# Kernel optimization log

Hardware: AMD Instinct MI355X
Metric: run time of the kernel (lower is better)

The kernel has to match this reference:

```python
import jax, jax.numpy as jnp
import numpy as np

N_NODES = 100000
N_EDGES = 1600000
IN_DIM = 768
HIDDEN = 256
N_CLASSES = 3


def setup_inputs() -> dict:
    key = jax.random.key(0)
    k0, k1, k2, k3 = jax.random.split(key, 4)
    x = jax.random.normal(k0, (N_NODES, IN_DIM), dtype=jnp.float32)
    edge_index = jax.random.randint(k1, (2, N_EDGES), 0, N_NODES, dtype=jnp.int32)
    # Glorot-ish init for weights
    W1 = jax.random.normal(k2, (IN_DIM, HIDDEN), dtype=jnp.float32) * (1.0 / np.sqrt(IN_DIM))
    b1 = jnp.zeros((HIDDEN,), dtype=jnp.float32)
    W2 = jax.random.normal(k3, (HIDDEN, N_CLASSES), dtype=jnp.float32) * (1.0 / np.sqrt(HIDDEN))
    b2 = jnp.zeros((N_CLASSES,), dtype=jnp.float32)
    return {"x": x, "edge_index": edge_index, "W1": W1, "b1": b1, "W2": W2, "b2": b2}


def reference(x, edge_index, W1, b1, W2, b2):
    """dumb_GNN forward: GCNConv(768->H) -> relu -> (dropout=eval identity) -> Linear -> log_softmax.

    GCNConv math (PyG default): out = D^{-1/2} (A + I) D^{-1/2} X W + b
    """
    n = x.shape[0]
    src, dst = edge_index[0], edge_index[1]
    # add self-loops
    loops = jnp.arange(n, dtype=src.dtype)
    src = jnp.concatenate([src, loops])
    dst = jnp.concatenate([dst, loops])
    # symmetric degree normalization (degrees include self-loops)
    deg = jax.ops.segment_sum(jnp.ones_like(src, dtype=x.dtype), dst, num_segments=n)
    dinv = jnp.where(deg > 0, jax.lax.rsqrt(deg), jnp.zeros_like(deg))
    norm = dinv[src] * dinv[dst]  # [E+N]
    # transform then gather-scale-scatter aggregate
    h = x @ W1  # [N, H]
    agg = jax.ops.segment_sum(h[src] * norm[:, None], dst, num_segments=n) + b1
    h = jax.nn.relu(agg)
    # dropout is identity at inference
    logits = h @ W2 + b2  # [N, C]
    return jax.nn.log_softmax(logits, axis=-1)
```

## Files before the change

### kernel.cpp

```cpp
#include <hip/hip_runtime.h>
#include <hip/hip_bf16.h>
#include <math.h>

#define N_NODES 100000
#define N_EDGES 1600000
#define IN_DIM  768
#define HIDDEN  256

#define SCAN_B  256
#define N_SBLK  ((N_NODES + SCAN_B - 1) / SCAN_B)

#define H_OFF    0ull
#define ADJ_OFF  51200000ull
#define RS_OFF   57600000ull
#define CUR_OFF  58000016ull
#define DEG_OFF  58400016ull
#define DINV_OFF 58800016ull
#define W1T_OFF  59200016ull
#define BSUM_OFF 59593232ull

typedef short          bf16x8 __attribute__((ext_vector_type(8)));
typedef float          fp32x4 __attribute__((ext_vector_type(4)));
typedef unsigned short u16x4  __attribute__((ext_vector_type(4)));

__device__ inline short f2bf(float f) {
    union { float f; unsigned u; } c; c.f = f;
    unsigned u = c.u;
    unsigned r = u + 0x7FFFu + ((u >> 16) & 1u);
    return (short)(r >> 16);
}

__device__ inline fp32x4 bf4_to_f4(u16x4 v) {
    fp32x4 r;
    for (int j = 0; j < 4; j++) {
        union { unsigned u; float f; } c;
        c.u = ((unsigned)v[j]) << 16;
        r[j] = c.f;
    }
    return r;
}

__global__ void init_kernel(int* __restrict__ deg, int* __restrict__ cursor) {
    int i = blockIdx.x * blockDim.x + threadIdx.x;
    if (i < N_NODES) { deg[i] = 0; cursor[i] = 0; }
}

__global__ void w1t_kernel(const float* __restrict__ w1, short* __restrict__ w1t) {
    int i = blockIdx.x * blockDim.x + threadIdx.x;
    if (i < HIDDEN * IN_DIM) {
        int n = i / IN_DIM, k = i % IN_DIM;
        w1t[i] = f2bf(w1[(size_t)k * HIDDEN + n]);
    }
}

__global__ void count_kernel(const int* __restrict__ dst, int* __restrict__ deg) {
    int e = blockIdx.x * blockDim.x + threadIdx.x;
    if (e < N_EDGES) atomicAdd(&deg[dst[e]], 1);
}

__global__ __launch_bounds__(SCAN_B) void scan1_kernel(const int* __restrict__ deg,
                                                       int* __restrict__ bsum) {
    int i = blockIdx.x * SCAN_B + threadIdx.x;
    int v = (i < N_NODES) ? deg[i] : 0;
    for (int off = 32; off > 0; off >>= 1) v += __shfl_down(v, off, 64);
    __shared__ int wsum[SCAN_B / 64];
    int lane = threadIdx.x & 63, w = threadIdx.x >> 6;
    if (lane == 0) wsum[w] = v;
    __syncthreads();
    if (threadIdx.x == 0) {
        int s = 0;
        for (int j = 0; j < SCAN_B / 64; j++) s += wsum[j];
        bsum[blockIdx.x] = s;
    }
}

__global__ __launch_bounds__(512) void scan2_kernel(int* __restrict__ bsum) {
    __shared__ int s[512];
    int tid = threadIdx.x;
    int v = (tid < N_SBLK) ? bsum[tid] : 0;
    s[tid] = v;
    __syncthreads();
    for (int off = 1; off < 512; off <<= 1) {
        int t = (tid >= off) ? s[tid - off] : 0;
        __syncthreads();
        s[tid] += t;
        __syncthreads();
    }
    if (tid < N_SBLK) bsum[tid] = s[tid] - v;
}

__global__ __launch_bounds__(SCAN_B) void scan3_kernel(const int* __restrict__ deg,
                                                       const int* __restrict__ bsum,
                                                       int* __restrict__ row_start,
                                                       float* __restrict__ dinv) {
    __shared__ int s[SCAN_B];
    int i = blockIdx.x * SCAN_B + threadIdx.x;
    int tid = threadIdx.x;
    int d = (i < N_NODES) ? deg[i] : 0;
    s[tid] = d;
    __syncthreads();
    for (int off = 1; off < SCAN_B; off <<= 1) {
        int t = (tid >= off) ? s[tid - off] : 0;
        __syncthreads();
        s[tid] += t;
        __syncthreads();
    }
    if (i < N_NODES) {
        row_start[i] = bsum[blockIdx.x] + s[tid] - d;
        dinv[i] = rsqrtf((float)(d + 1));
        if (i == N_NODES - 1) row_start[N_NODES] = N_EDGES;
    }
}

__global__ void fill_kernel(const int* __restrict__ src, const int* __restrict__ dst,
                            const int* __restrict__ row_start, int* __restrict__ cursor,
                            int* __restrict__ adj) {
    int e = blockIdx.x * blockDim.x + threadIdx.x;
    if (e < N_EDGES) {
        int d = dst[e];
        int p = row_start[d] + atomicAdd(&cursor[d], 1);
        adj[p] = src[e];
    }
}

__global__ __launch_bounds__(256) void gemm1_kernel(const float* __restrict__ x,
                                                    const short* __restrict__ w1t,
                                                    const float* __restrict__ dinv,
                                                    unsigned short* __restrict__ h) {
    __shared__ short a_lds[128][40];
    __shared__ short b_lds[128][40];

    const int tid  = threadIdx.x;
    const int lane = tid & 63;
    const int wave = tid >> 6;
    const int wm = (wave >> 1) * 64;
    const int wn = (wave & 1) * 64;
    const int l15 = lane & 15;
    const int q   = lane >> 4;
    const int row0 = blockIdx.x * 128;
    const int col0 = blockIdx.y * 128;

    const int sr0 = tid >> 2;
    const int sr1 = 64 + (tid >> 2);
    const int skk = (tid & 3) * 8;
    const int gr0 = row0 + sr0;
    const int gr1 = row0 + sr1;
    const float* xp0 = x + (size_t)gr0 * IN_DIM + skk;
    const float* xp1 = x + (size_t)gr1 * IN_DIM + skk;
    const short* wp0 = w1t + (size_t)(col0 + sr0) * IN_DIM + skk;
    const short* wp1 = w1t + (size_t)(col0 + sr1) * IN_DIM + skk;
    const bool ok0 = gr0 < N_NODES;
    const bool ok1 = gr1 < N_NODES;

    fp32x4 acc[4][4];
    for (int i = 0; i < 4; i++)
        for (int j = 0; j < 4; j++)
            for (int r = 0; r < 4; r++) acc[i][j][r] = 0.0f;

    fp32x4 pa0a = {0,0,0,0}, pa0b = {0,0,0,0}, pa1a = {0,0,0,0}, pa1b = {0,0,0,0};
    bf16x8 pb0, pb1;

    if (ok0) { pa0a = *(const fp32x4*)xp0; pa0b = *(const fp32x4*)(xp0 + 4); }
    if (ok1) { pa1a = *(const fp32x4*)xp1; pa1b = *(const fp32x4*)(xp1 + 4); }
    pb0 = *(const bf16x8*)wp0;
    pb1 = *(const bf16x8*)wp1;

    for (int k0 = 0; k0 < IN_DIM; k0 += 32) {
        bf16x8 av;
        av[0] = f2bf(pa0a[0]); av[1] = f2bf(pa0a[1]);
        av[2] = f2bf(pa0a[2]); av[3] = f2bf(pa0a[3]);
        av[4] = f2bf(pa0b[0]); av[5] = f2bf(pa0b[1]);
        av[6] = f2bf(pa0b[2]); av[7] = f2bf(pa0b[3]);
        *(bf16x8*)(&a_lds[sr0][skk]) = av;
        av[0] = f2bf(pa1a[0]); av[1] = f2bf(pa1a[1]);
        av[2] = f2bf(pa1a[2]); av[3] = f2bf(pa1a[3]);
        av[4] = f2bf(pa1b[0]); av[5] = f2bf(pa1b[1]);
        av[6] = f2bf(pa1b[2]); av[7] = f2bf(pa1b[3]);
        *(bf16x8*)(&a_lds[sr1][skk]) = av;
        *(bf16x8*)(&b_lds[sr0][skk]) = pb0;
        *(bf16x8*)(&b_lds[sr1][skk]) = pb1;
        __syncthreads();

        int kn = k0 + 32;
        if (kn < IN_DIM) {
            if (ok0) { pa0a = *(const fp32x4*)(xp0 + kn); pa0b = *(const fp32x4*)(xp0 + kn + 4); }
            if (ok1) { pa1a = *(const fp32x4*)(xp1 + kn); pa1b = *(const fp32x4*)(xp1 + kn + 4); }
            pb0 = *(const bf16x8*)(wp0 + kn);
            pb1 = *(const bf16x8*)(wp1 + kn);
        }

        bf16x8 af[4], bfr[4];
        for (int mt = 0; mt < 4; mt++)
            af[mt] = *(const bf16x8*)(&a_lds[wm + mt * 16 + l15][q * 8]);
        for (int nt = 0; nt < 4; nt++)
            bfr[nt] = *(const bf16x8*)(&b_lds[wn + nt * 16 + l15][q * 8]);
        for (int mt = 0; mt < 4; mt++)
            for (int nt = 0; nt < 4; nt++)
                acc[mt][nt] = __builtin_amdgcn_mfma_f32_16x16x32_bf16(
                    af[mt], bfr[nt], acc[mt][nt], 0, 0, 0);
        __syncthreads();
    }

    float dv[4][4];
    for (int mt = 0; mt < 4; mt++)
        for (int r = 0; r < 4; r++) {
            int row = row0 + wm + mt * 16 + q * 4 + r;
            dv[mt][r] = (row < N_NODES) ? dinv[row] : 0.0f;
        }
    for (int mt = 0; mt < 4; mt++) {
        for (int nt = 0; nt < 4; nt++) {
            int col = col0 + wn + nt * 16 + l15;
            for (int r = 0; r < 4; r++) {
                int row = row0 + wm + mt * 16 + q * 4 + r;
                if (row < N_NODES)
                    h[(size_t)row * HIDDEN + col] =
                        (unsigned short)f2bf(dv[mt][r] * acc[mt][nt][r]);
            }
        }
    }
}

__global__ __launch_bounds__(256) void aggregate_kernel(
    const unsigned short* __restrict__ h, const int* __restrict__ adj,
    const int* __restrict__ row_start, const float* __restrict__ dinv,
    const float* __restrict__ b1, const float* __restrict__ w2,
    const float* __restrict__ b2, float* __restrict__ out) {
    const int lane = threadIdx.x & 63;
    const int wave = threadIdx.x >> 6;
    const int v = blockIdx.x * 4 + wave;
    if (v >= N_NODES) return;

    const size_t loff = (size_t)lane * 4;

    fp32x4 a0 = bf4_to_f4(*(const u16x4*)(h + (size_t)v * HIDDEN + loff));
    fp32x4 a1 = {0,0,0,0}, a2 = {0,0,0,0}, a3 = {0,0,0,0};

    int e0 = row_start[v], e1 = row_start[v + 1];
    for (int e = e0; e < e1; e += 64) {
        int cnt = min(64, e1 - e);
        int s = (lane < cnt) ? adj[e + lane] : 0;
        int i = 0;
        for (; i + 4 <= cnt; i += 4) {
            int s0 = __shfl(s, i,     64);
            int s1 = __shfl(s, i + 1, 64);
            int s2 = __shfl(s, i + 2, 64);
            int s3 = __shfl(s, i + 3, 64);
            u16x4 r0 = *(const u16x4*)(h + (size_t)s0 * HIDDEN + loff);
            u16x4 r1 = *(const u16x4*)(h + (size_t)s1 * HIDDEN + loff);
            u16x4 r2 = *(const u16x4*)(h + (size_t)s2 * HIDDEN + loff);
            u16x4 r3 = *(const u16x4*)(h + (size_t)s3 * HIDDEN + loff);
            a0 += bf4_to_f4(r0);
            a1 += bf4_to_f4(r1);
            a2 += bf4_to_f4(r2);
            a3 += bf4_to_f4(r3);
        }
        for (; i < cnt; i++) {
            int si = __shfl(s, i, 64);
            a0 += bf4_to_f4(*(const u16x4*)(h + (size_t)si * HIDDEN + loff));
        }
    }
    fp32x4 acc = (a0 + a1) + (a2 + a3);

    float dvv = dinv[v];
    fp32x4 bb = *(const fp32x4*)(b1 + loff);
    float hr[4];
    for (int j = 0; j < 4; j++) hr[j] = fmaxf(0.0f, dvv * acc[j] + bb[j]);

    float p0 = 0.f, p1 = 0.f, p2 = 0.f;
    for (int j = 0; j < 4; j++) {
        const float* wr = w2 + (size_t)(lane * 4 + j) * 3;
        p0 += hr[j] * wr[0];
        p1 += hr[j] * wr[1];
        p2 += hr[j] * wr[2];
    }
    for (int off = 32; off > 0; off >>= 1) {
        p0 += __shfl_down(p0, off, 64);
        p1 += __shfl_down(p1, off, 64);
        p2 += __shfl_down(p2, off, 64);
    }
    if (lane == 0) {
        p0 += b2[0]; p1 += b2[1]; p2 += b2[2];
        float m = fmaxf(p0, fmaxf(p1, p2));
        float l = logf(expf(p0 - m) + expf(p1 - m) + expf(p2 - m));
        out[(size_t)v * 3 + 0] = p0 - m - l;
        out[(size_t)v * 3 + 1] = p1 - m - l;
        out[(size_t)v * 3 + 2] = p2 - m - l;
    }
}

extern "C" void kernel_launch(void* const* d_in, const int* in_sizes, int n_in,
                              void* d_out, int out_size, void* d_ws, size_t ws_size,
                              hipStream_t stream) {
    const float* x    = (const float*)d_in[0];
    const int*   ei   = (const int*)d_in[1];
    const float* W1   = (const float*)d_in[2];
    const float* b1   = (const float*)d_in[3];
    const float* W2   = (const float*)d_in[4];
    const float* b2   = (const float*)d_in[5];
    float* out = (float*)d_out;

    const int* src = ei;
    const int* dst = ei + N_EDGES;

    char* ws = (char*)d_ws;
    unsigned short* h_ws = (unsigned short*)(ws + H_OFF);
    int*   adj       = (int*)(ws + ADJ_OFF);
    int*   row_start = (int*)(ws + RS_OFF);
    int*   cursor    = (int*)(ws + CUR_OFF);
    int*   deg       = (int*)(ws + DEG_OFF);
    float* dinv      = (float*)(ws + DINV_OFF);
    short* w1t       = (short*)(ws + W1T_OFF);
    int*   bsum      = (int*)(ws + BSUM_OFF);

    init_kernel<<<(N_NODES + 255) / 256, 256, 0, stream>>>(deg, cursor);
    w1t_kernel<<<(HIDDEN * IN_DIM + 255) / 256, 256, 0, stream>>>(W1, w1t);
    count_kernel<<<(N_EDGES + 255) / 256, 256, 0, stream>>>(dst, deg);
    scan1_kernel<<<N_SBLK, SCAN_B, 0, stream>>>(deg, bsum);
    scan2_kernel<<<1, 512, 0, stream>>>(bsum);
    scan3_kernel<<<N_SBLK, SCAN_B, 0, stream>>>(deg, bsum, row_start, dinv);
    fill_kernel<<<(N_EDGES + 255) / 256, 256, 0, stream>>>(src, dst, row_start, cursor, adj);
    gemm1_kernel<<<dim3((N_NODES + 127) / 128, HIDDEN / 128), 256, 0, stream>>>(x, w1t, dinv, h_ws);
    aggregate_kernel<<<N_NODES / 4, 256, 0, stream>>>(h_ws, adj, row_start, dinv, b1, W2, b2, out);
}
```

Before: 771.7 us.

## Double-buffer GEMM tiles with direct global-to-LDS loads; half-wave aggregation

The GEMM now double-buffers its LDS tiles, loading W1t straight into LDS with global_load_lds and converting the next x tile after the MFMAs, so each k-step needs one barrier instead of two. The LDS layout becomes k-chunk-major with no padding. The aggregation kernel handles two nodes per wave, one per 32-lane half, each lane gathering 16-byte bf16 rows, to cut shuffle and reduction overhead and widen the loads. The unpadded LDS layout may cause bank conflicts, and the wider per-lane data raises register use.

```diff
diff --git a/kernel.cpp b/kernel.cpp
--- a/kernel.cpp
+++ b/kernel.cpp
@@ -21,7 +21,8 @@
 
 typedef short          bf16x8 __attribute__((ext_vector_type(8)));
 typedef float          fp32x4 __attribute__((ext_vector_type(4)));
-typedef unsigned short u16x4  __attribute__((ext_vector_type(4)));
+typedef float          fp32x8 __attribute__((ext_vector_type(8)));
+typedef unsigned short u16x8  __attribute__((ext_vector_type(8)));
 
 __device__ inline short f2bf(float f) {
     union { float f; unsigned u; } c; c.f = f;
@@ -30,14 +31,20 @@
     return (short)(r >> 16);
 }
 
-__device__ inline fp32x4 bf4_to_f4(u16x4 v) {
-    fp32x4 r;
-    for (int j = 0; j < 4; j++) {
+__device__ inline fp32x8 bf8_to_f8(u16x8 v) {
+    fp32x8 r;
+    for (int j = 0; j < 8; j++) {
         union { unsigned u; float f; } c;
         c.u = ((unsigned)v[j]) << 16;
         r[j] = c.f;
     }
     return r;
+}
+
+__device__ inline void gl_lds16(const short* g, short* l) {
+    __builtin_amdgcn_global_load_lds(
+        (const __attribute__((address_space(1))) unsigned int*)g,
+        (__attribute__((address_space(3))) unsigned int*)l, 16, 0, 0);
 }
 
 __global__ void init_kernel(int* __restrict__ deg, int* __restrict__ cursor) {
@@ -127,8 +134,8 @@
                                                     const short* __restrict__ w1t,
                                                     const float* __restrict__ dinv,
                                                     unsigned short* __restrict__ h) {
-    __shared__ short a_lds[128][40];
-    __shared__ short b_lds[128][40];
+    __shared__ __attribute__((aligned(16))) short a_lds[2][4096];
+    __shared__ __attribute__((aligned(16))) short b_lds[2][4096];
 
     const int tid  = threadIdx.x;
     const int lane = tid & 63;
@@ -140,65 +147,82 @@
     const int row0 = blockIdx.x * 128;
     const int col0 = blockIdx.y * 128;
 
-    const int sr0 = tid >> 2;
-    const int sr1 = 64 + (tid >> 2);
-    const int skk = (tid & 3) * 8;
-    const int gr0 = row0 + sr0;
-    const int gr1 = row0 + sr1;
-    const float* xp0 = x + (size_t)gr0 * IN_DIM + skk;
-    const float* xp1 = x + (size_t)gr1 * IN_DIM + skk;
-    const short* wp0 = w1t + (size_t)(col0 + sr0) * IN_DIM + skk;
-    const short* wp1 = w1t + (size_t)(col0 + sr1) * IN_DIM + skk;
-    const bool ok0 = gr0 < N_NODES;
-    const bool ok1 = gr1 < N_NODES;
+    const int arow = tid & 127;
+    const int aq   = (tid >> 7) * 2;
+    const int agr  = row0 + arow;
+    const bool aok = agr < N_NODES;
+    const float* axp = x + (size_t)agr * IN_DIM + aq * 8;
+
+    const int bslot0 = wave * 64 + lane;
+    const int bslot1 = 256 + wave * 64 + lane;
+    const short* bgp0 = w1t + (size_t)(col0 + (bslot0 & 127)) * IN_DIM + (bslot0 >> 7) * 8;
+    const short* bgp1 = w1t + (size_t)(col0 + (bslot1 & 127)) * IN_DIM + (bslot1 >> 7) * 8;
+    short* const bl0base0 = &b_lds[0][(size_t)(wave * 64) * 8];
+    short* const bl0base1 = &b_lds[0][(size_t)(256 + wave * 64) * 8];
+    short* const bl1base0 = &b_lds[1][(size_t)(wave * 64) * 8];
+    short* const bl1base1 = &b_lds[1][(size_t)(256 + wave * 64) * 8];
 
     fp32x4 acc[4][4];
     for (int i = 0; i < 4; i++)
         for (int j = 0; j < 4; j++)
             for (int r = 0; r < 4; r++) acc[i][j][r] = 0.0f;
 
-    fp32x4 pa0a = {0,0,0,0}, pa0b = {0,0,0,0}, pa1a = {0,0,0,0}, pa1b = {0,0,0,0};
-    bf16x8 pb0, pb1;
-
-    if (ok0) { pa0a = *(const fp32x4*)xp0; pa0b = *(const fp32x4*)(xp0 + 4); }
-    if (ok1) { pa1a = *(const fp32x4*)xp1; pa1b = *(const fp32x4*)(xp1 + 4); }
-    pb0 = *(const bf16x8*)wp0;
-    pb1 = *(const bf16x8*)wp1;
-
+    gl_lds16(bgp0, bl0base0);
+    gl_lds16(bgp1, bl0base1);
+    {
+        fp32x4 p0 = {0,0,0,0}, p1 = {0,0,0,0}, p2 = {0,0,0,0}, p3 = {0,0,0,0};
+        if (aok) {
+            p0 = *(const fp32x4*)axp;       p1 = *(const fp32x4*)(axp + 4);
+            p2 = *(const fp32x4*)(axp + 8); p3 = *(const fp32x4*)(axp + 12);
+        }
+        bf16x8 av;
+        av[0]=f2bf(p0[0]); av[1]=f2bf(p0[1]); av[2]=f2bf(p0[2]); av[3]=f2bf(p0[3]);
+        av[4]=f2bf(p1[0]); av[5]=f2bf(p1[1]); av[6]=f2bf(p1[2]); av[7]=f2bf(p1[3]);
+        *(bf16x8*)(&a_lds[0][(size_t)(aq * 128 + arow) * 8]) = av;
+        av[0]=f2bf(p2[0]); av[1]=f2bf(p2[1]); av[2]=f2bf(p2[2]); av[3]=f2bf(p2[3]);
+        av[4]=f2bf(p3[0]); av[5]=f2bf(p3[1]); av[6]=f2bf(p3[2]); av[7]=f2bf(p3[3]);
+        *(bf16x8*)(&a_lds[0][(size_t)((aq + 1) * 128 + arow) * 8]) = av;
+    }
+
+    int cur = 0;
     for (int k0 = 0; k0 < IN_DIM; k0 += 32) {
-        bf16x8 av;
-        av[0] = f2bf(pa0a[0]); av[1] = f2bf(pa0a[1]);
-        av[2] = f2bf(pa0a[2]); av[3] = f2bf(pa0a[3]);
-        av[4] = f2bf(pa0b[0]); av[5] = f2bf(pa0b[1]);
-        av[6] = f2bf(pa0b[2]); av[7] = f2bf(pa0b[3]);
-        *(bf16x8*)(&a_lds[sr0][skk]) = av;
-        av[0] = f2bf(pa1a[0]); av[1] = f2bf(pa1a[1]);
-        av[2] = f2bf(pa1a[2]); av[3] = f2bf(pa1a[3]);
-        av[4] = f2bf(pa1b[0]); av[5] = f2bf(pa1b[1]);
-        av[6] = f2bf(pa1b[2]); av[7] = f2bf(pa1b[3]);
-        *(bf16x8*)(&a_lds[sr1][skk]) = av;
-        *(bf16x8*)(&b_lds[sr0][skk]) = pb0;
-        *(bf16x8*)(&b_lds[sr1][skk]) = pb1;
-        __syncthreads();
-
-        int kn = k0 + 32;
-        if (kn < IN_DIM) {
-            if (ok0) { pa0a = *(const fp32x4*)(xp0 + kn); pa0b = *(const fp32x4*)(xp0 + kn + 4); }
-            if (ok1) { pa1a = *(const fp32x4*)(xp1 + kn); pa1b = *(const fp32x4*)(xp1 + kn + 4); }
-            pb0 = *(const bf16x8*)(wp0 + kn);
-            pb1 = *(const bf16x8*)(wp1 + kn);
+        __syncthreads();
+        const int nxt = cur ^ 1;
+        const bool more = (k0 + 32) < IN_DIM;
+
+        fp32x4 p0, p1, p2, p3;
+        if (more) {
+            gl_lds16(bgp0 + k0 + 32, nxt ? bl1base0 : bl0base0);
+            gl_lds16(bgp1 + k0 + 32, nxt ? bl1base1 : bl0base1);
+            if (aok) {
+                const float* p = axp + k0 + 32;
+                p0 = *(const fp32x4*)p;       p1 = *(const fp32x4*)(p + 4);
+                p2 = *(const fp32x4*)(p + 8); p3 = *(const fp32x4*)(p + 12);
+            } else {
+                p0 = p1 = p2 = p3 = (fp32x4){0,0,0,0};
+            }
         }
 
         bf16x8 af[4], bfr[4];
         for (int mt = 0; mt < 4; mt++)
-            af[mt] = *(const bf16x8*)(&a_lds[wm + mt * 16 + l15][q * 8]);
+            af[mt] = *(const bf16x8*)(&a_lds[cur][(size_t)(q * 128 + wm + mt * 16 + l15) * 8]);
         for (int nt = 0; nt < 4; nt++)
-            bfr[nt] = *(const bf16x8*)(&b_lds[wn + nt * 16 + l15][q * 8]);
+            bfr[nt] = *(const bf16x8*)(&b_lds[cur][(size_t)(q * 128 + wn + nt * 16 + l15) * 8]);
         for (int mt = 0; mt < 4; mt++)
             for (int nt = 0; nt < 4; nt++)
                 acc[mt][nt] = __builtin_amdgcn_mfma_f32_16x16x32_bf16(
                     af[mt], bfr[nt], acc[mt][nt], 0, 0, 0);
-        __syncthreads();
+
+        if (more) {
+            bf16x8 av;
+            av[0]=f2bf(p0[0]); av[1]=f2bf(p0[1]); av[2]=f2bf(p0[2]); av[3]=f2bf(p0[3]);
+            av[4]=f2bf(p1[0]); av[5]=f2bf(p1[1]); av[6]=f2bf(p1[2]); av[7]=f2bf(p1[3]);
+            *(bf16x8*)(&a_lds[nxt][(size_t)(aq * 128 + arow) * 8]) = av;
+            av[0]=f2bf(p2[0]); av[1]=f2bf(p2[1]); av[2]=f2bf(p2[2]); av[3]=f2bf(p2[3]);
+            av[4]=f2bf(p3[0]); av[5]=f2bf(p3[1]); av[6]=f2bf(p3[2]); av[7]=f2bf(p3[3]);
+            *(bf16x8*)(&a_lds[nxt][(size_t)((aq + 1) * 128 + arow) * 8]) = av;
+        }
+        cur = nxt;
     }
 
     float dv[4][4];
@@ -227,58 +251,59 @@
     const float* __restrict__ b2, float* __restrict__ out) {
     const int lane = threadIdx.x & 63;
     const int wave = threadIdx.x >> 6;
-    const int v = blockIdx.x * 4 + wave;
-    if (v >= N_NODES) return;
-
-    const size_t loff = (size_t)lane * 4;
-
-    fp32x4 a0 = bf4_to_f4(*(const u16x4*)(h + (size_t)v * HIDDEN + loff));
-    fp32x4 a1 = {0,0,0,0}, a2 = {0,0,0,0}, a3 = {0,0,0,0};
+    const int half = lane >> 5;
+    const int l32  = lane & 31;
+    const int v = blockIdx.x * 8 + wave * 2 + half;
+
+    const size_t choff = (size_t)l32 * 8;
+
+    fp32x8 a0 = bf8_to_f8(*(const u16x8*)(h + (size_t)v * HIDDEN + choff));
+    fp32x8 a1 = {0,0,0,0,0,0,0,0}, a2 = a1, a3 = a1;
 
     int e0 = row_start[v], e1 = row_start[v + 1];
-    for (int e = e0; e < e1; e += 64) {
-        int cnt = min(64, e1 - e);
-        int s = (lane < cnt) ? adj[e + lane] : 0;
+    for (int e = e0; e < e1; e += 32) {
+        int cnt = min(32, e1 - e);
+        int s = (l32 < cnt) ? adj[e + l32] : 0;
         int i = 0;
         for (; i + 4 <= cnt; i += 4) {
-            int s0 = __shfl(s, i,     64);
-            int s1 = __shfl(s, i + 1, 64);
-            int s2 = __shfl(s, i + 2, 64);
-            int s3 = __shfl(s, i + 3, 64);
-            u16x4 r0 = *(const u16x4*)(h + (size_t)s0 * HIDDEN + loff);
-            u16x4 r1 = *(const u16x4*)(h + (size_t)s1 * HIDDEN + loff);
-            u16x4 r2 = *(const u16x4*)(h + (size_t)s2 * HIDDEN + loff);
-            u16x4 r3 = *(const u16x4*)(h + (size_t)s3 * HIDDEN + loff);
-            a0 += bf4_to_f4(r0);
-            a1 += bf4_to_f4(r1);
-            a2 += bf4_to_f4(r2);
-            a3 += bf4_to_f4(r3);
+            int s0 = __shfl(s, i,     32);
+            int s1 = __shfl(s, i + 1, 32);
+            int s2 = __shfl(s, i + 2, 32);
+            int s3 = __shfl(s, i + 3, 32);
+            u16x8 r0 = *(const u16x8*)(h + (size_t)s0 * HIDDEN + choff);
+            u16x8 r1 = *(const u16x8*)(h + (size_t)s1 * HIDDEN + choff);
+            u16x8 r2 = *(const u16x8*)(h + (size_t)s2 * HIDDEN + choff);
+            u16x8 r3 = *(const u16x8*)(h + (size_t)s3 * HIDDEN + choff);
+            a0 += bf8_to_f8(r0);
+            a1 += bf8_to_f8(r1);
+            a2 += bf8_to_f8(r2);
+            a3 += bf8_to_f8(r3);
         }
         for (; i < cnt; i++) {
-            int si = __shfl(s, i, 64);
-            a0 += bf4_to_f4(*(const u16x4*)(h + (size_t)si * HIDDEN + loff));
-        }
-    }
-    fp32x4 acc = (a0 + a1) + (a2 + a3);
+            int si = __shfl(s, i, 32);
+            a0 += bf8_to_f8(*(const u16x8*)(h + (size_t)si * HIDDEN + choff));
+        }
+    }
+    fp32x8 acc = (a0 + a1) + (a2 + a3);
 
     float dvv = dinv[v];
-    fp32x4 bb = *(const fp32x4*)(b1 + loff);
-    float hr[4];
-    for (int j = 0; j < 4; j++) hr[j] = fmaxf(0.0f, dvv * acc[j] + bb[j]);
+    float hr[8];
+    for (int j = 0; j < 8; j++)
+        hr[j] = fmaxf(0.0f, dvv * acc[j] + b1[choff + j]);
 
     float p0 = 0.f, p1 = 0.f, p2 = 0.f;
-    for (int j = 0; j < 4; j++) {
-        const float* wr = w2 + (size_t)(lane * 4 + j) * 3;
+    for (int j = 0; j < 8; j++) {
+        const float* wr = w2 + (choff + j) * 3;
         p0 += hr[j] * wr[0];
         p1 += hr[j] * wr[1];
         p2 += hr[j] * wr[2];
     }
-    for (int off = 32; off > 0; off >>= 1) {
-        p0 += __shfl_down(p0, off, 64);
-        p1 += __shfl_down(p1, off, 64);
-        p2 += __shfl_down(p2, off, 64);
-    }
-    if (lane == 0) {
+    for (int off = 16; off > 0; off >>= 1) {
+        p0 += __shfl_down(p0, off, 32);
+        p1 += __shfl_down(p1, off, 32);
+        p2 += __shfl_down(p2, off, 32);
+    }
+    if (l32 == 0) {
         p0 += b2[0]; p1 += b2[1]; p2 += b2[2];
         float m = fmaxf(p0, fmaxf(p1, p2));
         float l = logf(expf(p0 - m) + expf(p1 - m) + expf(p2 - m));
@@ -320,5 +345,5 @@
     scan3_kernel<<<N_SBLK, SCAN_B, 0, stream>>>(deg, bsum, row_start, dinv);
     fill_kernel<<<(N_EDGES + 255) / 256, 256, 0, stream>>>(src, dst, row_start, cursor, adj);
     gemm1_kernel<<<dim3((N_NODES + 127) / 128, HIDDEN / 128), 256, 0, stream>>>(x, w1t, dinv, h_ws);
-    aggregate_kernel<<<N_NODES / 4, 256, 0, stream>>>(h_ws, adj, row_start, dinv, b1, W2, b2, out);
-}
+    aggregate_kernel<<<N_NODES / 8, 256, 0, stream>>>(h_ws, adj, row_start, dinv, b1, W2, b2, out);
+}
```

Result: slower. 826.4 us (+7.1%).
